# Kernel tuning notes

Measured on AMD Instinct MI355X. Metric: run time of the kernel, lower is better.

## Reference

```python
import jax, jax.numpy as jnp
import numpy as np

B, T, D_IN, H, NUM_CLASSES = 1024, 512, 4, 64, 3
G = 4 * H  # gates: i, f, g, o (PyTorch order)


def setup_inputs() -> dict:
    key = jax.random.key(0)
    ks = jax.random.split(key, 32)
    s = 0.1  # small init scale, like PyTorch's 1/sqrt(H) uniform
    inp = {"x": jax.random.normal(ks[0], (B, T, D_IN), jnp.float32)}
    i = 1
    for l in range(4):
        d = D_IN if l == 0 else H
        inp[f"w_ih_{l}"] = s * jax.random.normal(ks[i], (G, d), jnp.float32); i += 1
        inp[f"w_hh_{l}"] = s * jax.random.normal(ks[i], (G, H), jnp.float32); i += 1
        inp[f"b_ih_{l}"] = s * jax.random.normal(ks[i], (G,), jnp.float32); i += 1
        inp[f"b_hh_{l}"] = s * jax.random.normal(ks[i], (G,), jnp.float32); i += 1
    inp["fc1_w"] = s * jax.random.normal(ks[i], (H // 2, H), jnp.float32); i += 1
    inp["fc1_b"] = s * jax.random.normal(ks[i], (H // 2,), jnp.float32); i += 1
    inp["fc2_w"] = s * jax.random.normal(ks[i], (NUM_CLASSES, H // 2), jnp.float32); i += 1
    inp["fc2_b"] = s * jax.random.normal(ks[i], (NUM_CLASSES,), jnp.float32)
    return inp


def _lstm_layer(x, w_ih, w_hh, b_ih, b_hh):
    # x: [B, T, d_in] -> [B, T, H]; PyTorch gate order i, f, g, o.
    b, t, _ = x.shape
    # Precompute input contribution for all timesteps in one GEMM.
    pre = jnp.einsum('btd,gd->tbg', x, w_ih) + (b_ih + b_hh)  # [T, B, 4H]
    h0 = jnp.zeros((b, H), x.dtype)
    c0 = jnp.zeros((b, H), x.dtype)

    def step(carry, p):
        h, c = carry
        gates = p + h @ w_hh.T  # [B, 4H]
        i_g, f_g, g_g, o_g = jnp.split(gates, 4, axis=-1)
        i_g = jax.nn.sigmoid(i_g)
        f_g = jax.nn.sigmoid(f_g)
        g_g = jnp.tanh(g_g)
        o_g = jax.nn.sigmoid(o_g)
        c = f_g * c + i_g * g_g
        h = o_g * jnp.tanh(c)
        return (h, c), h

    _, hs = jax.lax.scan(step, (h0, c0), pre)  # hs: [T, B, H]
    return hs.transpose(1, 0, 2)


def reference(x,
              w_ih_0, w_hh_0, b_ih_0, b_hh_0,
              w_ih_1, w_hh_1, b_ih_1, b_hh_1,
              w_ih_2, w_hh_2, b_ih_2, b_hh_2,
              w_ih_3, w_hh_3, b_ih_3, b_hh_3,
              fc1_w, fc1_b, fc2_w, fc2_b):
    layers = [(w_ih_0, w_hh_0, b_ih_0, b_hh_0),
              (w_ih_1, w_hh_1, b_ih_1, b_hh_1),
              (w_ih_2, w_hh_2, b_ih_2, b_hh_2),
              (w_ih_3, w_hh_3, b_ih_3, b_hh_3)]
    h = x
    for (wi, wh, bi, bh) in layers:
        h = _lstm_layer(h, wi, wh, bi, bh)
    last = h[:, -1, :]                         # [B, H]
    z = jax.nn.relu(last @ fc1_w.T + fc1_b)    # [B, H//2]
    logits = z @ fc2_w.T + fc2_b               # [B, 3]
    return jax.nn.softmax(logits, axis=1)
```

## Files before the change

### kernel.cpp

```cpp
#include <hip/hip_runtime.h>


#define TLEN 512
#define NCH  64
#define AG   __HIP_MEMORY_SCOPE_AGENT
#define SPIN_CAP 2000000
#define GATE 10

typedef __bf16 bf16x8 __attribute__((ext_vector_type(8)));
typedef float  f32x4  __attribute__((ext_vector_type(4)));

struct Params {
  const float* x;
  const float* wih[4]; const float* whh[4];
  const float* bih[4]; const float* bhh[4];
  const float* fc1w; const float* fc1b;
  const float* fc2w; const float* fc2b;
  float* out; char* ws;
  int CAP; int CM;
};

__device__ __forceinline__ bf16x8 bfzero() {
  union { unsigned long long u[2]; bf16x8 v; } z; z.u[0] = 0ull; z.u[1] = 0ull; return z.v;
}
__device__ __forceinline__ float fast_sigmoid(float x) {
  return __builtin_amdgcn_rcpf(1.f + __expf(-x));
}
__device__ __forceinline__ float fast_tanh(float x) {
  float e = __expf(2.f * x);
  return 1.f - 2.f * __builtin_amdgcn_rcpf(e + 1.f);
}
__device__ __forceinline__ void load_frag_pair(const unsigned short* sb, int l15, int quad,
                                               bf16x8& f0, bf16x8& f1) {
  const unsigned long long* a = (const unsigned long long*)(sb + l15 * 64 + quad * 8);
  const unsigned long long* b = (const unsigned long long*)(sb + l15 * 64 + 32 + quad * 8);
  union { bf16x8 v; unsigned long long u[2]; } c0, c1;
  c0.u[0] = __hip_atomic_load(&a[0], __ATOMIC_RELAXED, AG);
  c0.u[1] = __hip_atomic_load(&a[1], __ATOMIC_RELAXED, AG);
  c1.u[0] = __hip_atomic_load(&b[0], __ATOMIC_RELAXED, AG);
  c1.u[1] = __hip_atomic_load(&b[1], __ATOMIC_RELAXED, AG);
  f0 = c0.v; f1 = c1.v;
}

__global__ __launch_bounds__(512, 2) void lstm_split(Params p)
{
  const int bid   = blockIdx.x;
  const int role  = bid >> 6;
  const int chunk = bid & 63;
  const int b0    = chunk * 16;
  const int tid   = threadIdx.x;
  const int wave  = tid >> 6;
  const int grp   = wave >> 2;
  const int w     = wave & 3;
  const int lane  = tid & 63;
  const int quad  = lane >> 4;
  const int l15   = lane & 15;
  const int L     = role * 2 + grp;

  __shared__ __bf16 tiles[2][2][1024];
  __shared__ float  s_fc1w[2048];
  __shared__ float  s_z[512];
  __shared__ float  s_fc1b[32];
  __shared__ float  s_fc2w[96];
  __shared__ float  s_fc2b[3];

  int* flagp = (int*)p.ws + chunk * 16;
  int* ackp  = (int*)(p.ws + 16 * 1024) + chunk * 16;
  unsigned short* ringc = (unsigned short*)(p.ws + 32 * 1024) + (size_t)chunk * p.CAP * 1024;
  const int CAP = p.CAP, CM = p.CM;

  bf16x8 wf[4][4];
  float  bias[4];
  {
    const float* wih = p.wih[L];
    const float* whh = p.whh[L];
    const float* bih = p.bih[L];
    const float* bhh = p.bhh[L];
#pragma unroll
    for (int g = 0; g < 4; g++) {
      int n = g * 64 + w * 16 + l15;
      bias[g] = bih[n] + bhh[n];
      if (L == 0) {
        bf16x8 f = bfzero();
        if (quad == 0) {
#pragma unroll
          for (int j = 0; j < 4; j++) f[j] = (__bf16)wih[n * 4 + j];
        }
        wf[g][0] = f; wf[g][1] = bfzero();
      } else {
#pragma unroll
        for (int q = 0; q < 2; q++) {
          const float* s = wih + n * 64 + q * 32 + quad * 8;
          bf16x8 f;
#pragma unroll
          for (int j = 0; j < 8; j++) f[j] = (__bf16)s[j];
          wf[g][q] = f;
        }
      }
#pragma unroll
      for (int q = 0; q < 2; q++) {
        const float* s = whh + n * 64 + q * 32 + quad * 8;
        bf16x8 f;
#pragma unroll
        for (int j = 0; j < 8; j++) f[j] = (__bf16)s[j];
        wf[g][2 + q] = f;
      }
    }
  }

  { int* ti = (int*)tiles; for (int i = tid; i < 2048; i += 512) ti[i] = 0; }
  float cst[4] = {0.f, 0.f, 0.f, 0.f};

  int W = -1000000000, f_pend = -1000000000;
  int ackW = -1000000000, a_pend = -1000000000;
  bf16x8 xA0 = bfzero(), xA1 = bfzero();
  bf16x8 xB0 = bfzero(), xB1 = bfzero();
  bf16x8 xC0 = bfzero(), xC1 = bfzero();
  float4 xraw = {0.f, 0.f, 0.f, 0.f};

  if (role == 0) {
    if (grp == 0 && quad == 0) {
      const float* xb = p.x + (size_t)(b0 + l15) * TLEN * 4;
      const float4 x0 = *(const float4*)(xb);
      const float4 x1 = *(const float4*)(xb + 4);
      xraw = *(const float4*)(xb + 8);
      bf16x8 f = bfzero();
      f[0] = (__bf16)x0.x; f[1] = (__bf16)x0.y; f[2] = (__bf16)x0.z; f[3] = (__bf16)x0.w;
      xA0 = f;
      bf16x8 g = bfzero();
      g[0] = (__bf16)x1.x; g[1] = (__bf16)x1.y; g[2] = (__bf16)x1.z; g[3] = (__bf16)x1.w;
      xB0 = g;
    }
  } else if (grp == 0) {
    int v = -1000000000, it = 0;
    do {
      if (lane == 0) v = __hip_atomic_load(flagp, __ATOMIC_ACQUIRE, AG);
      v = __shfl(v, 0);
      if (v >= GATE) break;
      __builtin_amdgcn_s_sleep(1);
    } while (++it < SPIN_CAP);
    W = v;
    load_frag_pair(ringc,        l15, quad, xA0, xA1);
    load_frag_pair(ringc + 1024, l15, quad, xB0, xB1);
    load_frag_pair(ringc + 2048, l15, quad, xC0, xC1);
  }
  __syncthreads();

  const int SMAX = (role == 0) ? (TLEN + 2) : (TLEN + 1);
  for (int s = 0; s < SMAX; s++) {
    const int t  = s - grp;
    const int pr = s & 1, pw = pr ^ 1;
    unsigned hb[4];

    if ((unsigned)t < (unsigned)TLEN) {
      bf16x8 if0, if1;
      if (grp == 0) { if0 = xA0; if1 = xA1; }
      else {
        const __bf16* src = tiles[pr][0];
        int sg0 = quad ^ (l15 & 7);
        int sg1 = (4 + quad) ^ (l15 & 7);
        if0 = *(const bf16x8*)&src[l15 * 64 + sg0 * 8];
        if1 = *(const bf16x8*)&src[l15 * 64 + sg1 * 8];
      }
      bf16x8 hf0, hf1;
      {
        const __bf16* src = tiles[pr][grp];
        int sg0 = quad ^ (l15 & 7);
        int sg1 = (4 + quad) ^ (l15 & 7);
        hf0 = *(const bf16x8*)&src[l15 * 64 + sg0 * 8];
        hf1 = *(const bf16x8*)&src[l15 * 64 + sg1 * 8];
      }

      f32x4 acc[4];
#pragma unroll
      for (int g = 0; g < 4; g++) { f32x4 a = {bias[g], bias[g], bias[g], bias[g]}; acc[g] = a; }
      if (L == 0) {
#pragma unroll
        for (int g = 0; g < 4; g++)
          acc[g] = __builtin_amdgcn_mfma_f32_16x16x32_bf16(if0, wf[g][0], acc[g], 0, 0, 0);
      } else {
#pragma unroll
        for (int g = 0; g < 4; g++) {
          acc[g] = __builtin_amdgcn_mfma_f32_16x16x32_bf16(if0, wf[g][0], acc[g], 0, 0, 0);
          acc[g] = __builtin_amdgcn_mfma_f32_16x16x32_bf16(if1, wf[g][1], acc[g], 0, 0, 0);
        }
      }
#pragma unroll
      for (int g = 0; g < 4; g++) {
        acc[g] = __builtin_amdgcn_mfma_f32_16x16x32_bf16(hf0, wf[g][2], acc[g], 0, 0, 0);
        acc[g] = __builtin_amdgcn_mfma_f32_16x16x32_bf16(hf1, wf[g][3], acc[g], 0, 0, 0);
      }

      const int col = w * 16 + l15;
      __bf16* dst = tiles[pw][grp];
#pragma unroll
      for (int r = 0; r < 4; r++) {
        float ig = fast_sigmoid(acc[0][r]);
        float fg = fast_sigmoid(acc[1][r]);
        float gg = fast_tanh(acc[2][r]);
        float og = fast_sigmoid(acc[3][r]);
        float c = fg * cst[r] + ig * gg;
        cst[r] = c;
        float h = og * fast_tanh(c);
        __bf16 hbf = (__bf16)h;
        union { __bf16 b; unsigned short s; } cv; cv.b = hbf;
        hb[r] = cv.s;
        int m  = quad * 4 + r;
        int sg = (col >> 3) ^ (m & 7);
        dst[m * 64 + sg * 8 + (col & 7)] = hbf;
      }
    }

    __syncthreads();

    if (role == 0) {
      if (grp == 0) {
        xA0 = xB0;
        if (quad == 0) {
          bf16x8 f = bfzero();
          f[0] = (__bf16)xraw.x; f[1] = (__bf16)xraw.y;
          f[2] = (__bf16)xraw.z; f[3] = (__bf16)xraw.w;
          xB0 = f;
          if (t + 3 < TLEN)
            xraw = *(const float4*)(p.x + ((size_t)(b0 + l15) * TLEN + (t + 3)) * 4);
        }
      }
      if (grp == 1 && (unsigned)t < (unsigned)TLEN) {
        int am = __shfl(a_pend, 0);
        if (am > ackW) ackW = am;
        if (lane == 0) a_pend = __hip_atomic_load(ackp, __ATOMIC_RELAXED, AG);
        if (t >= CAP && ackW < t - CAP + 1) {
          int v = ackW, it = 0;
          do {
            if (lane == 0) v = __hip_atomic_load(ackp, __ATOMIC_ACQUIRE, AG);
            v = __shfl(v, 0);
            if (v >= t - CAP + 1) break;
            __builtin_amdgcn_s_sleep(1);
          } while (++it < SPIN_CAP);
          ackW = v;
        }
        const int col = w * 16 + l15;
        unsigned* rdst = (unsigned*)(ringc + (size_t)(t & CM) * 1024);
#pragma unroll
        for (int r = 0; r < 4; r++) {
          unsigned v = hb[r];
          unsigned o = (unsigned)__shfl_xor((int)v, 1);
          if ((lane & 1) == 0) {
            int m = quad * 4 + r;
            __hip_atomic_store(&rdst[(m * 64 + col) >> 1], v | (o << 16), __ATOMIC_RELAXED, AG);
          }
        }
      }
      if (tid == 0 && s >= 2)
        __hip_atomic_store(flagp, s - 1, __ATOMIC_RELAXED, AG);
    } else {
      if (grp == 0) {
        int fm = __shfl(f_pend, 0);
        if (fm > W) W = fm;
        if (lane == 0) f_pend = __hip_atomic_load(flagp, __ATOMIC_RELAXED, AG);
        xA0 = xB0; xA1 = xB1; xB0 = xC0; xB1 = xC1;
        if (t + 3 < TLEN) {
          if (W < t + 4) {
            int v = W, it = 0;
            do {
              if (lane == 0) v = __hip_atomic_load(flagp, __ATOMIC_ACQUIRE, AG);
              v = __shfl(v, 0);
              if (v >= t + 4) break;
              __builtin_amdgcn_s_sleep(1);
            } while (++it < SPIN_CAP);
            W = v;
          }
          load_frag_pair(ringc + (size_t)((t + 3) & CM) * 1024, l15, quad, xC0, xC1);
        }
      }
      if (tid == 0)
        __hip_atomic_store(ackp, s + 2, __ATOMIC_RELAXED, AG);
    }
  }

  if (role == 1) {
    for (int i = tid; i < 2048; i += 512) s_fc1w[i] = p.fc1w[i];
    if (tid < 32) s_fc1b[tid] = p.fc1b[tid];
    if (tid < 96) s_fc2w[tid] = p.fc2w[tid];
    if (tid < 3)  s_fc2b[tid] = p.fc2b[tid];
    __syncthreads();
    {
      int m = tid >> 5, u = tid & 31;
      float sacc = s_fc1b[u];
      const float* wrow = &s_fc1w[u * 64];
      const __bf16* hfin = tiles[1][1];
#pragma unroll
      for (int k = 0; k < 64; k++) {
        int sg = (k >> 3) ^ (m & 7);
        sacc += (float)hfin[m * 64 + sg * 8 + (k & 7)] * wrow[k];
      }
      s_z[m * 32 + u] = fmaxf(sacc, 0.f);
    }
    __syncthreads();
    if (tid < 16) {
      int m = tid;
      float lg[3];
#pragma unroll
      for (int v = 0; v < 3; v++) {
        float sv = s_fc2b[v];
#pragma unroll
        for (int u = 0; u < 32; u++) sv += s_z[m * 32 + u] * s_fc2w[v * 32 + u];
        lg[v] = sv;
      }
      float mx = fmaxf(lg[0], fmaxf(lg[1], lg[2]));
      float e0 = __expf(lg[0] - mx), e1 = __expf(lg[1] - mx), e2 = __expf(lg[2] - mx);
      float inv = 1.f / (e0 + e1 + e2);
      float* o = p.out + (size_t)(b0 + m) * 3;
      o[0] = e0 * inv; o[1] = e1 * inv; o[2] = e2 * inv;
    }
  }
}

__global__ __launch_bounds__(1024) void lstm_fused(Params p)
{
  const int chunk = blockIdx.x;
  const int b0   = chunk * 16;
  const int tid  = threadIdx.x;
  const int wave = tid >> 6;
  const int L    = wave >> 2;
  const int w    = wave & 3;
  const int lane = tid & 63;
  const int quad = lane >> 4;
  const int l15  = lane & 15;

  __shared__ __bf16 tiles[2][5][16 * 64];
  __shared__ float  s_fc1w[2048];
  __shared__ float  s_z[512];
  __shared__ float  s_fc1b[32];
  __shared__ float  s_fc2w[96];
  __shared__ float  s_fc2b[3];

  bf16x8 wf[4][4];
  float  bias[4];
  {
    const float* wih = p.wih[L];
    const float* whh = p.whh[L];
    const float* bih = p.bih[L];
    const float* bhh = p.bhh[L];
#pragma unroll
    for (int g = 0; g < 4; g++) {
      int n = g * 64 + w * 16 + l15;
      bias[g] = bih[n] + bhh[n];
      if (L == 0) {
        bf16x8 f = bfzero();
        if (quad == 0) {
#pragma unroll
          for (int j = 0; j < 4; j++) f[j] = (__bf16)wih[n * 4 + j];
        }
        wf[g][0] = f; wf[g][1] = bfzero();
      } else {
#pragma unroll
        for (int q = 0; q < 2; q++) {
          const float* s = wih + n * 64 + q * 32 + quad * 8;
          bf16x8 f;
#pragma unroll
          for (int j = 0; j < 8; j++) f[j] = (__bf16)s[j];
          wf[g][q] = f;
        }
      }
#pragma unroll
      for (int q = 0; q < 2; q++) {
        const float* s = whh + n * 64 + q * 32 + quad * 8;
        bf16x8 f;
#pragma unroll
        for (int j = 0; j < 8; j++) f[j] = (__bf16)s[j];
        wf[g][2 + q] = f;
      }
    }
  }

  { int* ti = (int*)tiles; for (int i = tid; i < 5120; i += 1024) ti[i] = 0; }
  float cst[4] = {0.f, 0.f, 0.f, 0.f};

  if (wave == 0 && quad == 0) {
    const float4 xv = *(const float4*)(p.x + ((size_t)(b0 + l15) * TLEN) * 4);
    __bf16 v[4] = {(__bf16)xv.x, (__bf16)xv.y, (__bf16)xv.z, (__bf16)xv.w};
    *(float2*)&tiles[0][0][l15 * 64 + (l15 & 7) * 8] = *(float2*)v;
  }
  __syncthreads();

  for (int s = 0; s < TLEN + 3; s++) {
    const int t  = s - L;
    const int pr = s & 1;
    const int pw = pr ^ 1;

    if ((unsigned)t < (unsigned)TLEN) {
      const __bf16* in  = tiles[pr][L];
      const __bf16* own = tiles[pr][L + 1];
      const int sg0 = quad ^ (l15 & 7);
      const int sg1 = (4 + quad) ^ (l15 & 7);
      bf16x8 xf0 = *(const bf16x8*)&in [l15 * 64 + sg0 * 8];
      bf16x8 xf1 = *(const bf16x8*)&in [l15 * 64 + sg1 * 8];
      bf16x8 hf0 = *(const bf16x8*)&own[l15 * 64 + sg0 * 8];
      bf16x8 hf1 = *(const bf16x8*)&own[l15 * 64 + sg1 * 8];

      f32x4 acc[4];
#pragma unroll
      for (int g = 0; g < 4; g++) { f32x4 a = {bias[g], bias[g], bias[g], bias[g]}; acc[g] = a; }
#pragma unroll
      for (int g = 0; g < 4; g++) {
        acc[g] = __builtin_amdgcn_mfma_f32_16x16x32_bf16(xf0, wf[g][0], acc[g], 0, 0, 0);
        acc[g] = __builtin_amdgcn_mfma_f32_16x16x32_bf16(xf1, wf[g][1], acc[g], 0, 0, 0);
        acc[g] = __builtin_amdgcn_mfma_f32_16x16x32_bf16(hf0, wf[g][2], acc[g], 0, 0, 0);
        acc[g] = __builtin_amdgcn_mfma_f32_16x16x32_bf16(hf1, wf[g][3], acc[g], 0, 0, 0);
      }

      if (wave == 0 && quad == 0 && t + 1 < TLEN) {
        const float4 xv = *(const float4*)(p.x + ((size_t)(b0 + l15) * TLEN + (t + 1)) * 4);
        __bf16 v[4] = {(__bf16)xv.x, (__bf16)xv.y, (__bf16)xv.z, (__bf16)xv.w};
        *(float2*)&tiles[pw][0][l15 * 64 + (l15 & 7) * 8] = *(float2*)v;
      }

      const int col = w * 16 + l15;
      __bf16* dst = tiles[pw][L + 1];
#pragma unroll
      for (int r = 0; r < 4; r++) {
        float ig = fast_sigmoid(acc[0][r]);
        float fg = fast_sigmoid(acc[1][r]);
        float gg = fast_tanh(acc[2][r]);
        float og = fast_sigmoid(acc[3][r]);
        float c = fg * cst[r] + ig * gg;
        cst[r] = c;
        float h = og * fast_tanh(c);
        int m  = quad * 4 + r;
        int sg = (col >> 3) ^ (m & 7);
        dst[m * 64 + sg * 8 + (col & 7)] = (__bf16)h;
      }
    }
    __syncthreads();
  }

  for (int i = tid; i < 2048; i += 1024) s_fc1w[i] = p.fc1w[i];
  if (tid < 32) s_fc1b[tid] = p.fc1b[tid];
  if (tid < 96) s_fc2w[tid] = p.fc2w[tid];
  if (tid < 3)  s_fc2b[tid] = p.fc2b[tid];
  __syncthreads();
  if (tid < 512) {
    int m = tid >> 5, u = tid & 31;
    float sacc = s_fc1b[u];
    const float* wrow = &s_fc1w[u * 64];
    const __bf16* hfin = tiles[1][4];
#pragma unroll
    for (int k = 0; k < 64; k++) {
      int sg = (k >> 3) ^ (m & 7);
      sacc += (float)hfin[m * 64 + sg * 8 + (k & 7)] * wrow[k];
    }
    s_z[m * 32 + u] = fmaxf(sacc, 0.f);
  }
  __syncthreads();
  if (tid < 16) {
    int m = tid;
    float lg[3];
#pragma unroll
    for (int v = 0; v < 3; v++) {
      float sv = s_fc2b[v];
#pragma unroll
      for (int u = 0; u < 32; u++) sv += s_z[m * 32 + u] * s_fc2w[v * 32 + u];
      lg[v] = sv;
    }
    float mx = fmaxf(lg[0], fmaxf(lg[1], lg[2]));
    float e0 = __expf(lg[0] - mx), e1 = __expf(lg[1] - mx), e2 = __expf(lg[2] - mx);
    float inv = 1.f / (e0 + e1 + e2);
    float* o = p.out + (size_t)(b0 + m) * 3;
    o[0] = e0 * inv; o[1] = e1 * inv; o[2] = e2 * inv;
  }
}

extern "C" void kernel_launch(void* const* d_in, const int* in_sizes, int n_in,
                              void* d_out, int out_size, void* d_ws, size_t ws_size,
                              hipStream_t stream)
{
  (void)in_sizes; (void)n_in; (void)out_size;
  Params p;
  p.x = (const float*)d_in[0];
  for (int l = 0; l < 4; l++) {
    p.wih[l] = (const float*)d_in[1 + 4 * l];
    p.whh[l] = (const float*)d_in[2 + 4 * l];
    p.bih[l] = (const float*)d_in[3 + 4 * l];
    p.bhh[l] = (const float*)d_in[4 + 4 * l];
  }
  p.fc1w = (const float*)d_in[17];
  p.fc1b = (const float*)d_in[18];
  p.fc2w = (const float*)d_in[19];
  p.fc2b = (const float*)d_in[20];
  p.out = (float*)d_out;
  p.ws  = (char*)d_ws;

  const size_t avail = (ws_size > 32768) ? (ws_size - 32768) : 0;
  int CAP = 1;
  while (CAP < 64 && (size_t)(CAP * 2) * (NCH * 2048ull) <= avail) CAP <<= 1;

  if (CAP >= 16) {
    p.CAP = CAP; p.CM = CAP - 1;
    hipLaunchKernelGGL(lstm_split, dim3(128), dim3(512), 0, stream, p);
  } else {
    p.CAP = 0; p.CM = 0;
    hipLaunchKernelGGL(lstm_fused, dim3(NCH), dim3(1024), 0, stream, p);
  }
}
```

Baseline: 881.4 us.

## Pipeline LSTM layers across four workgroups per batch chunk via ring buffers

Adds a new kernel that gives each of the four LSTM layers its own 256-thread workgroup per 16-row batch chunk, 256 blocks in total. Layers hand h_t to the next layer through global ring buffers guarded by flag and ack counters, replacing the previous two-layers-per-block split. Gate pre-activations are folded into log2e-scaled weights so exp2 can be used directly. It also makes the startup gate depth a runtime parameter. This spreads the serial recurrence over more CUs, at the cost of more cross-workgroup spin-wait synchronization and global memory traffic per step.

```diff
diff --git a/kernel.cpp b/kernel.cpp
--- a/kernel.cpp
+++ b/kernel.cpp
@@ -5,7 +5,8 @@
 #define NCH  64
 #define AG   __HIP_MEMORY_SCOPE_AGENT
 #define SPIN_CAP 2000000
-#define GATE 10
+#define LOG2E 1.44269504f
+#define TWOLOG2E 2.88539008f
 
 typedef __bf16 bf16x8 __attribute__((ext_vector_type(8)));
 typedef float  f32x4  __attribute__((ext_vector_type(4)));
@@ -17,7 +18,7 @@
   const float* fc1w; const float* fc1b;
   const float* fc2w; const float* fc2b;
   float* out; char* ws;
-  int CAP; int CM;
+  int CAP; int CM; int D;
 };
 
 __device__ __forceinline__ bf16x8 bfzero() {
@@ -42,6 +43,274 @@
   f0 = c0.v; f1 = c1.v;
 }
 
+__global__ __launch_bounds__(256, 1) void lstm_pipe4(Params p)
+{
+  const int bid   = blockIdx.x;
+  const int L     = bid & 3;
+  const int chunk = bid >> 2;
+  const int b0    = chunk * 16;
+  const int tid   = threadIdx.x;
+  const int w     = tid >> 6;
+  const int lane  = tid & 63;
+  const int quad  = lane >> 4;
+  const int l15   = lane & 15;
+
+  __shared__ __bf16 hown[2][1024];
+  __shared__ float  s_fc1w[2048];
+  __shared__ float  s_z[512];
+  __shared__ float  s_fc1b[32];
+  __shared__ float  s_fc2w[96];
+  __shared__ float  s_fc2b[3];
+
+  const int CAP = p.CAP, CM = p.CM, GATE = p.D;
+  int* flags = (int*)p.ws;
+  int* acks  = (int*)(p.ws + 12 * 1024);
+  unsigned short* ringbase = (unsigned short*)(p.ws + 32 * 1024);
+  const int bsrc = (L > 0) ? (L - 1) : 0;
+  int* flag_src = flags + (bsrc * 64 + chunk) * 16;
+  int* ack_src  = acks  + (bsrc * 64 + chunk) * 16;
+  int* flag_dst = flags + (L * 64 + chunk) * 16;
+  int* ack_dst  = acks  + (L * 64 + chunk) * 16;
+  const unsigned short* ring_src = ringbase + (size_t)(bsrc * 64 + chunk) * CAP * 1024;
+  unsigned short*       ring_dst = (unsigned short*)ringbase + (size_t)(L * 64 + chunk) * CAP * 1024;
+
+  bf16x8 wf[4][4];
+  float  bias[4];
+  {
+    const float gsc[4] = { -LOG2E, -LOG2E, TWOLOG2E, -LOG2E };
+    const float* wih = p.wih[L];
+    const float* whh = p.whh[L];
+    const float* bih = p.bih[L];
+    const float* bhh = p.bhh[L];
+#pragma unroll
+    for (int g = 0; g < 4; g++) {
+      const float sc = gsc[g];
+      int n = g * 64 + w * 16 + l15;
+      bias[g] = (bih[n] + bhh[n]) * sc;
+      if (L == 0) {
+        bf16x8 f = bfzero();
+        if (quad == 0) {
+#pragma unroll
+          for (int j = 0; j < 4; j++) f[j] = (__bf16)(wih[n * 4 + j] * sc);
+        }
+        wf[g][0] = f; wf[g][1] = bfzero();
+      } else {
+#pragma unroll
+        for (int q = 0; q < 2; q++) {
+          const float* s = wih + n * 64 + q * 32 + quad * 8;
+          bf16x8 f;
+#pragma unroll
+          for (int j = 0; j < 8; j++) f[j] = (__bf16)(s[j] * sc);
+          wf[g][q] = f;
+        }
+      }
+#pragma unroll
+      for (int q = 0; q < 2; q++) {
+        const float* s = whh + n * 64 + q * 32 + quad * 8;
+        bf16x8 f;
+#pragma unroll
+        for (int j = 0; j < 8; j++) f[j] = (__bf16)(s[j] * sc);
+        wf[g][2 + q] = f;
+      }
+    }
+  }
+
+  { int* hi = (int*)hown; for (int i = tid; i < 1024; i += 256) hi[i] = 0; }
+  float cst[4] = {0.f, 0.f, 0.f, 0.f};
+
+  int W = -1000000000, f_pend = -1000000000;
+  int ackW = -1000000000, a_pend = -1000000000;
+  bf16x8 xA0 = bfzero(), xA1 = bfzero();
+  bf16x8 xB0 = bfzero(), xB1 = bfzero();
+  bf16x8 xC0 = bfzero(), xC1 = bfzero();
+  float4 xraw = {0.f, 0.f, 0.f, 0.f};
+
+  if (L == 0) {
+    if (quad == 0) {
+      const float* xb = p.x + (size_t)(b0 + l15) * TLEN * 4;
+      const float4 x0 = *(const float4*)(xb);
+      const float4 x1 = *(const float4*)(xb + 4);
+      xraw = *(const float4*)(xb + 8);
+      bf16x8 f = bfzero();
+      f[0] = (__bf16)x0.x; f[1] = (__bf16)x0.y; f[2] = (__bf16)x0.z; f[3] = (__bf16)x0.w;
+      xA0 = f;
+      bf16x8 g = bfzero();
+      g[0] = (__bf16)x1.x; g[1] = (__bf16)x1.y; g[2] = (__bf16)x1.z; g[3] = (__bf16)x1.w;
+      xB0 = g;
+    }
+  } else {
+    int v = -1000000000, it = 0;
+    do {
+      if (lane == 0) v = __hip_atomic_load(flag_src, __ATOMIC_ACQUIRE, AG);
+      v = __shfl(v, 0);
+      if (v >= GATE) break;
+      __builtin_amdgcn_s_sleep(1);
+    } while (++it < SPIN_CAP);
+    W = v;
+    load_frag_pair(ring_src,        l15, quad, xA0, xA1);
+    load_frag_pair(ring_src + 1024, l15, quad, xB0, xB1);
+    load_frag_pair(ring_src + 2048, l15, quad, xC0, xC1);
+  }
+  __syncthreads();
+
+  const int SMAX = (L < 3) ? (TLEN + 2) : TLEN;
+  for (int s = 0; s < SMAX; s++) {
+    const int pr = s & 1, pw = pr ^ 1;
+    unsigned hb[4];
+
+    if (s < TLEN) {
+      bf16x8 hf0, hf1;
+      {
+        const __bf16* src = hown[pr];
+        int sg0 = quad ^ (l15 & 7);
+        int sg1 = (4 + quad) ^ (l15 & 7);
+        hf0 = *(const bf16x8*)&src[l15 * 64 + sg0 * 8];
+        hf1 = *(const bf16x8*)&src[l15 * 64 + sg1 * 8];
+      }
+      f32x4 acc[4];
+#pragma unroll
+      for (int g = 0; g < 4; g++) { f32x4 a = {bias[g], bias[g], bias[g], bias[g]}; acc[g] = a; }
+      if (L == 0) {
+#pragma unroll
+        for (int g = 0; g < 4; g++)
+          acc[g] = __builtin_amdgcn_mfma_f32_16x16x32_bf16(xA0, wf[g][0], acc[g], 0, 0, 0);
+      } else {
+#pragma unroll
+        for (int g = 0; g < 4; g++) {
+          acc[g] = __builtin_amdgcn_mfma_f32_16x16x32_bf16(xA0, wf[g][0], acc[g], 0, 0, 0);
+          acc[g] = __builtin_amdgcn_mfma_f32_16x16x32_bf16(xA1, wf[g][1], acc[g], 0, 0, 0);
+        }
+      }
+#pragma unroll
+      for (int g = 0; g < 4; g++) {
+        acc[g] = __builtin_amdgcn_mfma_f32_16x16x32_bf16(hf0, wf[g][2], acc[g], 0, 0, 0);
+        acc[g] = __builtin_amdgcn_mfma_f32_16x16x32_bf16(hf1, wf[g][3], acc[g], 0, 0, 0);
+      }
+
+      const int col = w * 16 + l15;
+      __bf16* dst = hown[pw];
+#pragma unroll
+      for (int r = 0; r < 4; r++) {
+        float ig = __builtin_amdgcn_rcpf(1.f + __builtin_amdgcn_exp2f(acc[0][r]));
+        float fg = __builtin_amdgcn_rcpf(1.f + __builtin_amdgcn_exp2f(acc[1][r]));
+        float gg = 1.f - 2.f * __builtin_amdgcn_rcpf(1.f + __builtin_amdgcn_exp2f(acc[2][r]));
+        float og = __builtin_amdgcn_rcpf(1.f + __builtin_amdgcn_exp2f(acc[3][r]));
+        float c  = fg * cst[r] + ig * gg;
+        cst[r] = c;
+        float th = 1.f - 2.f * __builtin_amdgcn_rcpf(1.f + __builtin_amdgcn_exp2f(TWOLOG2E * c));
+        float h  = og * th;
+        __bf16 hbf = (__bf16)h;
+        union { __bf16 b; unsigned short s; } cv; cv.b = hbf;
+        hb[r] = cv.s;
+        int m  = quad * 4 + r;
+        int sg = (col >> 3) ^ (m & 7);
+        dst[m * 64 + sg * 8 + (col & 7)] = hbf;
+      }
+    }
+
+    __syncthreads();
+
+    if (L > 0 && s < TLEN) {
+      int fm = __shfl(f_pend, 0);
+      if (fm > W) W = fm;
+      if (lane == 0) f_pend = __hip_atomic_load(flag_src, __ATOMIC_RELAXED, AG);
+      xA0 = xB0; xA1 = xB1; xB0 = xC0; xB1 = xC1;
+      if (tid == 0) __hip_atomic_store(ack_src, s + 2, __ATOMIC_RELAXED, AG);
+      if (s + 3 < TLEN) {
+        if (W < s + 4) {
+          int v = W, it = 0;
+          do {
+            if (lane == 0) v = __hip_atomic_load(flag_src, __ATOMIC_ACQUIRE, AG);
+            v = __shfl(v, 0);
+            if (v >= s + 4) break;
+            __builtin_amdgcn_s_sleep(1);
+          } while (++it < SPIN_CAP);
+          W = v;
+        }
+        load_frag_pair(ring_src + (size_t)((s + 3) & CM) * 1024, l15, quad, xC0, xC1);
+      }
+    }
+    if (L == 0 && s < TLEN) {
+      xA0 = xB0;
+      if (quad == 0) {
+        bf16x8 f = bfzero();
+        f[0] = (__bf16)xraw.x; f[1] = (__bf16)xraw.y;
+        f[2] = (__bf16)xraw.z; f[3] = (__bf16)xraw.w;
+        xB0 = f;
+        if (s + 3 < TLEN)
+          xraw = *(const float4*)(p.x + ((size_t)(b0 + l15) * TLEN + (s + 3)) * 4);
+      }
+    }
+    if (L < 3) {
+      if (s < TLEN) {
+        int am = __shfl(a_pend, 0);
+        if (am > ackW) ackW = am;
+        if (lane == 0) a_pend = __hip_atomic_load(ack_dst, __ATOMIC_RELAXED, AG);
+        if (s >= CAP && ackW < s - CAP + 1) {
+          int v = ackW, it = 0;
+          do {
+            if (lane == 0) v = __hip_atomic_load(ack_dst, __ATOMIC_ACQUIRE, AG);
+            v = __shfl(v, 0);
+            if (v >= s - CAP + 1) break;
+            __builtin_amdgcn_s_sleep(1);
+          } while (++it < SPIN_CAP);
+          ackW = v;
+        }
+        const int col = w * 16 + l15;
+        unsigned* rdst = (unsigned*)(ring_dst + (size_t)(s & CM) * 1024);
+#pragma unroll
+        for (int r = 0; r < 4; r++) {
+          unsigned v = hb[r];
+          unsigned o = (unsigned)__shfl_xor((int)v, 1);
+          if ((lane & 1) == 0) {
+            int m = quad * 4 + r;
+            __hip_atomic_store(&rdst[(m * 64 + col) >> 1], v | (o << 16), __ATOMIC_RELAXED, AG);
+          }
+        }
+      }
+      if (tid == 0 && s >= 1)
+        __hip_atomic_store(flag_dst, s - 1, __ATOMIC_RELAXED, AG);
+    }
+  }
+
+  if (L == 3) {
+    for (int i = tid; i < 2048; i += 256) s_fc1w[i] = p.fc1w[i];
+    if (tid < 32) s_fc1b[tid] = p.fc1b[tid];
+    if (tid < 96) s_fc2w[tid] = p.fc2w[tid];
+    if (tid < 3)  s_fc2b[tid] = p.fc2b[tid];
+    __syncthreads();
+    for (int pi = tid; pi < 512; pi += 256) {
+      int m = pi >> 5, u = pi & 31;
+      float sacc = s_fc1b[u];
+      const float* wrow = &s_fc1w[u * 64];
+      const __bf16* hfin = hown[0];
+#pragma unroll
+      for (int k = 0; k < 64; k++) {
+        int sg = (k >> 3) ^ (m & 7);
+        sacc += (float)hfin[m * 64 + sg * 8 + (k & 7)] * wrow[k];
+      }
+      s_z[m * 32 + u] = fmaxf(sacc, 0.f);
+    }
+    __syncthreads();
+    if (tid < 16) {
+      int m = tid;
+      float lg[3];
+#pragma unroll
+      for (int v = 0; v < 3; v++) {
+        float sv = s_fc2b[v];
+#pragma unroll
+        for (int u = 0; u < 32; u++) sv += s_z[m * 32 + u] * s_fc2w[v * 32 + u];
+        lg[v] = sv;
+      }
+      float mx = fmaxf(lg[0], fmaxf(lg[1], lg[2]));
+      float e0 = __expf(lg[0] - mx), e1 = __expf(lg[1] - mx), e2 = __expf(lg[2] - mx);
+      float inv = 1.f / (e0 + e1 + e2);
+      float* o = p.out + (size_t)(b0 + m) * 3;
+      o[0] = e0 * inv; o[1] = e1 * inv; o[2] = e2 * inv;
+    }
+  }
+}
+
 __global__ __launch_bounds__(512, 2) void lstm_split(Params p)
 {
   const int bid   = blockIdx.x;
@@ -136,7 +405,7 @@
     do {
       if (lane == 0) v = __hip_atomic_load(flagp, __ATOMIC_ACQUIRE, AG);
       v = __shfl(v, 0);
-      if (v >= GATE) break;
+      if (v >= 10) break;
       __builtin_amdgcn_s_sleep(1);
     } while (++it < SPIN_CAP);
     W = v;
@@ -492,14 +761,22 @@
   p.ws  = (char*)d_ws;
 
   const size_t avail = (ws_size > 32768) ? (ws_size - 32768) : 0;
+
+  int CAP4 = 1;
+  while (CAP4 < 16 && (size_t)(CAP4 * 2) * (3ull * NCH * 2048) <= avail) CAP4 <<= 1;
+  if (CAP4 >= 8) {
+    p.CAP = CAP4; p.CM = CAP4 - 1;
+    p.D = (CAP4 >= 16) ? 10 : 6;
+    hipLaunchKernelGGL(lstm_pipe4, dim3(256), dim3(256), 0, stream, p);
+    return;
+  }
   int CAP = 1;
   while (CAP < 64 && (size_t)(CAP * 2) * (NCH * 2048ull) <= avail) CAP <<= 1;
-
   if (CAP >= 16) {
-    p.CAP = CAP; p.CM = CAP - 1;
+    p.CAP = CAP; p.CM = CAP - 1; p.D = 10;
     hipLaunchKernelGGL(lstm_split, dim3(128), dim3(512), 0, stream, p);
-  } else {
-    p.CAP = 0; p.CM = 0;
-    hipLaunchKernelGGL(lstm_fused, dim3(NCH), dim3(1024), 0, stream, p);
-  }
+    return;
+  }
+  p.CAP = 0; p.CM = 0; p.D = 0;
+  hipLaunchKernelGGL(lstm_fused, dim3(NCH), dim3(1024), 0, stream, p);
 }
```

Result: slower. 1.061 ms (+20.4%).
